# Kernel optimization log

Measured on AMD Instinct MI355X. Metric: run time of the kernel, lower is better.

Reference implementation:

```python
import jax, jax.numpy as jnp
import numpy as np


def setup_inputs() -> dict:
    key = jax.random.key(0)
    kx, kk, kq, kv = jax.random.split(key, 4)
    B, T, C = 4, 2048, 1024
    scale = 1.0 / np.sqrt(C)
    x = jax.random.normal(kx, (B, T, C), dtype=jnp.float32)
    # nn.Linear(C, C, bias=False): y = x @ W.T, W is [C, C]
    Wk = jax.random.normal(kk, (C, C), dtype=jnp.float32) * scale
    Wq = jax.random.normal(kq, (C, C), dtype=jnp.float32) * scale
    Wv = jax.random.normal(kv, (C, C), dtype=jnp.float32) * scale
    return {"x": x, "Wk": Wk, "Wq": Wq, "Wv": Wv}


def reference(x, Wk, Wq, Wv):
    B, T, C = x.shape
    k = jnp.einsum('btc,dc->btd', x, Wk)  # [B,T,C]
    q = jnp.einsum('btc,dc->btd', x, Wq)
    v = jnp.einsum('btc,dc->btd', x, Wv)
    # full T x T score matrix, scaled by C**-0.5 (note: C, not head_dim split)
    wei = jnp.einsum('btd,bsd->bts', q, k) * (C ** -0.5)  # [B,T,T]
    causal = jnp.tril(jnp.ones((T, T), dtype=bool))
    wei = jnp.where(causal, wei, -jnp.inf)
    wei = jax.nn.softmax(wei, axis=-1)
    # dropout(p=0.1) omitted: reference is eval-mode (identity)
    out = jnp.einsum('bts,bsd->btd', wei, v)  # [B,T,C]
    return out
```

## Files before the change

kernel.cpp:

```cpp
#include <hip/hip_runtime.h>
#include <cstdio>
#include <cmath>

#define TSEQ 2048
#define CDIM 1024
#define NBATCH 4

typedef float f32x4 __attribute__((ext_vector_type(4)));
typedef __bf16 bf16x8 __attribute__((ext_vector_type(8)));
typedef unsigned short u16;

__device__ __forceinline__ u16 f2bf(float f) {
  unsigned u = __builtin_bit_cast(unsigned, f);
  unsigned r = (u + 0x7FFFu + ((u >> 16) & 1u)) >> 16;
  return (u16)r;
}

__device__ __forceinline__ void gload_lds16(const void* g, void* l) {
  __builtin_amdgcn_global_load_lds(
      (__attribute__((address_space(1))) void*)g,
      (__attribute__((address_space(3))) void*)l, 16, 0, 0);
}

#define SWZ2(b_) ((b_) ^ ((((b_) >> 7) & 7) << 4))

__device__ __forceinline__ void gemm128(
    const u16* __restrict__ A, const u16* __restrict__ B,
    int lda, int ldb, int m0, int n0, int nT,
    char* smem, f32x4 acc[4][4])
{
  u16* Ab = (u16*)smem;
  u16* Bb = (u16*)(smem + 32768);
  const int tid = threadIdx.x, w = tid >> 6, l = tid & 63;
  const int wr = w >> 1, wc = w & 1;
  const int frow = l & 15, fko = l >> 4;
  const int srow = l >> 3;
  const int scol = ((l & 7) * 8) ^ (((l >> 3) & 7) << 3);

  const u16* gA = A + (size_t)(m0 + w * 32 + srow) * lda + scol;
  const u16* gB = B + (size_t)(n0 + w * 32 + srow) * ldb + scol;

  auto stageA = [&](int t) {
    if (t >= nT) return;
    const u16* s = gA + t * 64;
    u16* d = Ab + (t & 1) * 8192 + w * 2048;
    gload_lds16(s, d);
    gload_lds16(s + (size_t)8 * lda, d + 512);
    gload_lds16(s + (size_t)16 * lda, d + 1024);
    gload_lds16(s + (size_t)24 * lda, d + 1536);
  };
  auto stageB = [&](int t) {
    if (t >= nT) return;
    const u16* s = gB + t * 64;
    u16* d = Bb + (t & 1) * 8192 + w * 2048;
    gload_lds16(s, d);
    gload_lds16(s + (size_t)8 * ldb, d + 512);
    gload_lds16(s + (size_t)16 * ldb, d + 1024);
    gload_lds16(s + (size_t)24 * ldb, d + 1536);
  };

#define AOFF(mf, ks) SWZ2(((wr * 64 + (mf) * 16 + frow) * 128 + (ks) * 64 + fko * 16))
#define BOFF(nf, ks) SWZ2(((wc * 64 + (nf) * 16 + frow) * 128 + (ks) * 64 + fko * 16))

  stageB(0); stageA(0); stageB(1); stageA(1);
  asm volatile("s_waitcnt vmcnt(8)" ::: "memory");
  __builtin_amdgcn_s_barrier();

#pragma unroll 1
  for (int t = 0; t < nT; ++t) {
    const char* Abase = (const char*)Ab + (t & 1) * 16384;
    const char* Bbase = (const char*)Bb + (t & 1) * 16384;
    bf16x8 bfr[4][2], af0[2][2];
#pragma unroll
    for (int nf = 0; nf < 4; ++nf)
#pragma unroll
      for (int ks = 0; ks < 2; ++ks)
        bfr[nf][ks] = *(const bf16x8*)(Bbase + BOFF(nf, ks));
#pragma unroll
    for (int mm = 0; mm < 2; ++mm)
#pragma unroll
      for (int ks = 0; ks < 2; ++ks)
        af0[mm][ks] = *(const bf16x8*)(Abase + AOFF(mm, ks));
    __builtin_amdgcn_sched_barrier(0);
    stageB(t + 2);
    __builtin_amdgcn_s_barrier();
    __builtin_amdgcn_s_setprio(1);
#pragma unroll
    for (int ks = 0; ks < 2; ++ks)
#pragma unroll
      for (int mm = 0; mm < 2; ++mm)
#pragma unroll
        for (int nf = 0; nf < 4; ++nf)
          acc[mm][nf] = __builtin_amdgcn_mfma_f32_16x16x32_bf16(
              af0[mm][ks], bfr[nf][ks], acc[mm][nf], 0, 0, 0);
    __builtin_amdgcn_s_setprio(0);
    __builtin_amdgcn_s_barrier();
    bf16x8 af1[2][2];
#pragma unroll
    for (int mm = 0; mm < 2; ++mm)
#pragma unroll
      for (int ks = 0; ks < 2; ++ks)
        af1[mm][ks] = *(const bf16x8*)(Abase + AOFF(2 + mm, ks));
    __builtin_amdgcn_sched_barrier(0);
    stageA(t + 2);
    __builtin_amdgcn_s_barrier();
    __builtin_amdgcn_s_setprio(1);
#pragma unroll
    for (int ks = 0; ks < 2; ++ks)
#pragma unroll
      for (int mm = 0; mm < 2; ++mm)
#pragma unroll
        for (int nf = 0; nf < 4; ++nf)
          acc[2 + mm][nf] = __builtin_amdgcn_mfma_f32_16x16x32_bf16(
              af1[mm][ks], bfr[nf][ks], acc[2 + mm][nf], 0, 0, 0);
    __builtin_amdgcn_s_setprio(0);
    if (t < nT - 2) asm volatile("s_waitcnt vmcnt(8)" ::: "memory");
    else if (t == nT - 2) asm volatile("s_waitcnt vmcnt(0)" ::: "memory");
    __builtin_amdgcn_s_barrier();
  }
#undef AOFF
#undef BOFF
}

#define ACC_ZERO4(acc)                                  \
  _Pragma("unroll") for (int m_ = 0; m_ < 4; ++m_)      \
  _Pragma("unroll") for (int n_ = 0; n_ < 4; ++n_)      \
      acc[m_][n_] = (f32x4){0.f, 0.f, 0.f, 0.f};

__global__ void __launch_bounds__(256) k_cvt_all(
    const float* __restrict__ x, const float* __restrict__ Wk,
    const float* __restrict__ Wq, const float* __restrict__ Wv,
    u16* __restrict__ xb, u16* __restrict__ wb)
{
  const int NX4 = (NBATCH * TSEQ * CDIM) / 4;
  const int NW4 = (CDIM * CDIM) / 4;
  int g = blockIdx.x * 256 + threadIdx.x;
  const float* src; u16* dst; int i;
  if (g < NX4) { src = x; dst = xb; i = g; }
  else {
    int g2 = g - NX4;
    int w = g2 / NW4; i = g2 - w * NW4;
    src = (w == 0) ? Wk : (w == 1) ? Wq : Wv;
    dst = wb + (size_t)w * CDIM * CDIM;
  }
  float4 v = ((const float4*)src)[i];
  ushort4 o;
  o.x = f2bf(v.x); o.y = f2bf(v.y); o.z = f2bf(v.z); o.w = f2bf(v.w);
  ((ushort4*)dst)[i] = o;
}

__global__ void __launch_bounds__(256, 2) k_gemm_qkv_t(
    const u16* __restrict__ xb, const u16* __restrict__ wb,
    u16* __restrict__ kb, u16* __restrict__ qb, u16* __restrict__ vt)
{
  extern __shared__ char smem[];
  const int id = blockIdx.x;
  const int xcd = id & 7, loc = id >> 3;
  const int mt = xcd * 8 + (loc & 7);
  const int nt = loc >> 3;
  const int m0 = mt * 128, n0g = nt * 128;

  f32x4 acc[4][4];
  ACC_ZERO4(acc);
  gemm128(xb, wb, CDIM, CDIM, m0, n0g, 16, smem, acc);

  const int tid = threadIdx.x, w = tid >> 6, l = tid & 63;
  const int wr = w >> 1, wc = w & 1;
  const int frow = l & 15, fko = l >> 4;
  const int z = n0g >> 10;
  if (z < 2) {
    u16* outp = (z == 0) ? kb : qb;
    const float scale = (z == 1) ? 0.03125f : 1.0f;
    const int r0 = m0 + wr * 64 + fko * 4;
    const int c0 = (n0g & 1023) + wc * 64 + frow;
#pragma unroll
    for (int mf = 0; mf < 4; ++mf)
#pragma unroll
      for (int nf = 0; nf < 4; ++nf) {
        const int r = r0 + mf * 16;
        const int c = c0 + nf * 16;
#pragma unroll
        for (int j = 0; j < 4; ++j)
          outp[(size_t)(r + j) * CDIM + c] = f2bf(acc[mf][nf][j] * scale);
      }
  } else {
    __syncthreads();
    u16* tile = (u16*)smem;
#pragma unroll
    for (int mf = 0; mf < 4; ++mf)
#pragma unroll
      for (int nf = 0; nf < 4; ++nf) {
        const int cl = wc * 64 + nf * 16 + frow;
        const int rl = wr * 64 + mf * 16 + fko * 4;
#pragma unroll
        for (int j = 0; j < 4; ++j)
          tile[cl * 136 + rl + j] = f2bf(acc[mf][nf][j]);
      }
    __syncthreads();
    const int b = m0 >> 11, t0 = m0 & 2047;
    const int c0g = n0g - 2048;
    u16* dst = vt + ((size_t)b * CDIM + c0g) * TSEQ + t0;
#pragma unroll
    for (int it = 0; it < 8; ++it) {
      const int idx = it * 256 + tid;
      const int c = idx >> 4, ch = idx & 15;
      bf16x8 v = *(const bf16x8*)(tile + c * 136 + ch * 8);
      *(bf16x8*)(dst + (size_t)c * TSEQ + ch * 8) = v;
    }
  }
}

__global__ void __launch_bounds__(256, 2) k_gemm_scores_t(
    const u16* __restrict__ qb, const u16* __restrict__ kb,
    u16* __restrict__ pb, float* __restrict__ rs)
{
  extern __shared__ char smem[];
  const int id = blockIdx.x;
  const int sw = (id & 7) * 68 + (id >> 3);
  const int b = sw / 136;
  const int wq = sw - b * 136;
  int y = (int)((sqrtf(8.f * wq + 1.f) - 1.f) * 0.5f);
  while ((y + 1) * (y + 2) / 2 <= wq) ++y;
  while (y * (y + 1) / 2 > wq) --y;
  const int xt = wq - y * (y + 1) / 2;
  const int m0 = y * 128, n0 = xt * 128;

  const u16* A = qb + (size_t)b * TSEQ * CDIM;
  const u16* B = kb + (size_t)b * TSEQ * CDIM;
  u16* P = pb + (size_t)b * TSEQ * TSEQ;

  f32x4 acc[4][4];
  ACC_ZERO4(acc);
  gemm128(A, B, CDIM, CDIM, m0, n0, 16, smem, acc);

  const int tid = threadIdx.x, w = tid >> 6, l = tid & 63;
  const int wr = w >> 1, wc = w & 1;
  const int frow = l & 15, fko = l >> 4;
  float* rowpart = (float*)smem;

#pragma unroll
  for (int mf = 0; mf < 4; ++mf) {
#pragma unroll
    for (int j = 0; j < 4; ++j) {
      const int rloc = wr * 64 + mf * 16 + fko * 4 + j;
      const int rglob = m0 + rloc;
      float p4 = 0.f;
#pragma unroll
      for (int nf = 0; nf < 4; ++nf) {
        const int c = n0 + wc * 64 + nf * 16 + frow;
        float e = (c <= rglob) ? __expf(acc[mf][nf][j]) : 0.f;
        p4 += e;
        P[(size_t)rglob * TSEQ + c] = f2bf(e);
      }
#pragma unroll
      for (int d = 1; d < 16; d <<= 1) p4 += __shfl_xor(p4, d);
      if (frow == 0) rowpart[rloc * 2 + wc] = p4;
    }
  }
  __syncthreads();
  if (tid < 128)
    rs[((size_t)b * 16 + xt) * TSEQ + m0 + tid] =
        rowpart[tid * 2] + rowpart[tid * 2 + 1];
}

__global__ void __launch_bounds__(256, 2) k_gemm_pv_t(
    const u16* __restrict__ pb, const u16* __restrict__ vt,
    const float* __restrict__ rs, float* __restrict__ out)
{
  extern __shared__ char smem[];
  const int id = blockIdx.x;
  const int n = id & 7, loc = id >> 3;
  const int b = loc >> 4, mt = loc & 15;
  const int m0 = mt * 128, n0 = n * 128;
  const int nT = 2 * (mt + 1);

  const u16* A = pb + (size_t)b * TSEQ * TSEQ;
  const u16* B = vt + (size_t)b * CDIM * TSEQ;
  float* O = out + (size_t)b * TSEQ * CDIM;

  f32x4 acc[4][4];
  ACC_ZERO4(acc);
  gemm128(A, B, TSEQ, TSEQ, m0, n0, nT, smem, acc);

  const int tid = threadIdx.x, w = tid >> 6, l = tid & 63;
  const int wr = w >> 1, wc = w & 1;
  const int frow = l & 15, fko = l >> 4;

  __syncthreads();
  float* sinv = (float*)smem;
  if (tid < 128) {
    float s = 0.f;
    const float* p = rs + (size_t)b * 16 * TSEQ + m0 + tid;
    for (int x = 0; x <= mt; ++x) s += p[(size_t)x * TSEQ];
    sinv[tid] = 1.f / s;
  }
  __syncthreads();

#pragma unroll
  for (int mf = 0; mf < 4; ++mf) {
    const int rloc = wr * 64 + mf * 16 + fko * 4;
    const int r = m0 + rloc;
    const float4 iv = *(const float4*)&sinv[rloc];
    const float ivj[4] = {iv.x, iv.y, iv.z, iv.w};
#pragma unroll
    for (int nf = 0; nf < 4; ++nf) {
      const int c = n0 + wc * 64 + nf * 16 + frow;
#pragma unroll
      for (int j = 0; j < 4; ++j)
        O[(size_t)(r + j) * CDIM + c] = acc[mf][nf][j] * ivj[j];
    }
  }
}

extern "C" void kernel_launch(void* const* d_in, const int* in_sizes, int n_in,
                              void* d_out, int out_size, void* d_ws, size_t ws_size,
                              hipStream_t stream) {
  const float* x  = (const float*)d_in[0];
  const float* Wk = (const float*)d_in[1];
  const float* Wq = (const float*)d_in[2];
  const float* Wv = (const float*)d_in[3];
  float* out = (float*)d_out;

  const size_t M = (size_t)NBATCH * TSEQ;

  size_t off = 0;
  auto alloc = [&](size_t bytes) {
    void* p = (char*)d_ws + off;
    off += (bytes + 255) & ~(size_t)255;
    return p;
  };
  u16* xb = (u16*)alloc(M * CDIM * 2);
  u16* wb = (u16*)alloc(3ull * CDIM * CDIM * 2);
  u16* qb = (u16*)alloc(M * CDIM * 2);
  u16* kb = (u16*)alloc(M * CDIM * 2);
  u16* vt = (u16*)alloc(M * CDIM * 2);
  u16* pbuf = (u16*)alloc((size_t)NBATCH * TSEQ * TSEQ * 2);
  float* rs = (float*)alloc((size_t)NBATCH * 16 * TSEQ * 4);
  if (off > ws_size) {
    fprintf(stderr, "kernel_launch: ws too small: need %zu, have %zu\n", off, ws_size);
    return;
  }

  const int NX4 = (NBATCH * TSEQ * CDIM) / 4;
  const int NW4 = (CDIM * CDIM) / 4;
  const int cvtBlocks = (NX4 + 3 * NW4) / 256;

  static_cast<void>(hipFuncSetAttribute(
      reinterpret_cast<const void*>(k_gemm_qkv_t),
      hipFuncAttributeMaxDynamicSharedMemorySize, 65536));
  static_cast<void>(hipFuncSetAttribute(
      reinterpret_cast<const void*>(k_gemm_scores_t),
      hipFuncAttributeMaxDynamicSharedMemorySize, 65536));
  static_cast<void>(hipFuncSetAttribute(
      reinterpret_cast<const void*>(k_gemm_pv_t),
      hipFuncAttributeMaxDynamicSharedMemorySize, 65536));

  k_cvt_all<<<cvtBlocks, 256, 0, stream>>>(x, Wk, Wq, Wv, xb, wb);
  k_gemm_qkv_t<<<1536, 256, 65536, stream>>>(xb, wb, kb, qb, vt);
  k_gemm_scores_t<<<544, 256, 65536, stream>>>(qb, kb, pbuf, rs);
  k_gemm_pv_t<<<512, 256, 65536, stream>>>(pbuf, vt, rs, out);
}
```

Measured before the change: 139.5 us.

## Simplify GEMM main loop and stage epilogue stores through LDS for coalescing

The gemm128 main loop is restructured from two half-phases, each with its own barrier and a prefetch issue, into one phase. Each iteration waits, loads all A and B fragments, runs all 32 MFMAs, then issues both next-tile prefetches after a single barrier. Separately, the QKV projection and scores kernels now write their bf16 outputs into an LDS tile and then store them with 16-byte coalesced vector writes, replacing scattered 2-byte global stores. This adds LDS traffic and extra syncs, and the new loop structure may reduce overlap of global loads with MFMA work.

Measured after the change: 135.9 us. -2.6%, faster.

```diff
diff --git a/kernel.cpp b/kernel.cpp
--- a/kernel.cpp
+++ b/kernel.cpp
@@ -63,60 +63,43 @@
 #define BOFF(nf, ks) SWZ2(((wc * 64 + (nf) * 16 + frow) * 128 + (ks) * 64 + fko * 16))
 
   stageB(0); stageA(0); stageB(1); stageA(1);
-  asm volatile("s_waitcnt vmcnt(8)" ::: "memory");
-  __builtin_amdgcn_s_barrier();
 
 #pragma unroll 1
   for (int t = 0; t < nT; ++t) {
+    if (t < nT - 1) asm volatile("s_waitcnt vmcnt(8)" ::: "memory");
+    else            asm volatile("s_waitcnt vmcnt(0)" ::: "memory");
+    __builtin_amdgcn_s_barrier();
+    __builtin_amdgcn_sched_barrier(0);
+
     const char* Abase = (const char*)Ab + (t & 1) * 16384;
     const char* Bbase = (const char*)Bb + (t & 1) * 16384;
-    bf16x8 bfr[4][2], af0[2][2];
+    bf16x8 bfr[4][2], afr[4][2];
 #pragma unroll
     for (int nf = 0; nf < 4; ++nf)
 #pragma unroll
       for (int ks = 0; ks < 2; ++ks)
         bfr[nf][ks] = *(const bf16x8*)(Bbase + BOFF(nf, ks));
 #pragma unroll
-    for (int mm = 0; mm < 2; ++mm)
+    for (int mf = 0; mf < 4; ++mf)
 #pragma unroll
       for (int ks = 0; ks < 2; ++ks)
-        af0[mm][ks] = *(const bf16x8*)(Abase + AOFF(mm, ks));
+        afr[mf][ks] = *(const bf16x8*)(Abase + AOFF(mf, ks));
+
+    __builtin_amdgcn_s_setprio(1);
+#pragma unroll
+    for (int ks = 0; ks < 2; ++ks)
+#pragma unroll
+      for (int mf = 0; mf < 4; ++mf)
+#pragma unroll
+        for (int nf = 0; nf < 4; ++nf)
+          acc[mf][nf] = __builtin_amdgcn_mfma_f32_16x16x32_bf16(
+              afr[mf][ks], bfr[nf][ks], acc[mf][nf], 0, 0, 0);
+    __builtin_amdgcn_s_setprio(0);
+
+    __builtin_amdgcn_s_barrier();
     __builtin_amdgcn_sched_barrier(0);
     stageB(t + 2);
-    __builtin_amdgcn_s_barrier();
-    __builtin_amdgcn_s_setprio(1);
-#pragma unroll
-    for (int ks = 0; ks < 2; ++ks)
-#pragma unroll
-      for (int mm = 0; mm < 2; ++mm)
-#pragma unroll
-        for (int nf = 0; nf < 4; ++nf)
-          acc[mm][nf] = __builtin_amdgcn_mfma_f32_16x16x32_bf16(
-              af0[mm][ks], bfr[nf][ks], acc[mm][nf], 0, 0, 0);
-    __builtin_amdgcn_s_setprio(0);
-    __builtin_amdgcn_s_barrier();
-    bf16x8 af1[2][2];
-#pragma unroll
-    for (int mm = 0; mm < 2; ++mm)
-#pragma unroll
-      for (int ks = 0; ks < 2; ++ks)
-        af1[mm][ks] = *(const bf16x8*)(Abase + AOFF(2 + mm, ks));
-    __builtin_amdgcn_sched_barrier(0);
     stageA(t + 2);
-    __builtin_amdgcn_s_barrier();
-    __builtin_amdgcn_s_setprio(1);
-#pragma unroll
-    for (int ks = 0; ks < 2; ++ks)
-#pragma unroll
-      for (int mm = 0; mm < 2; ++mm)
-#pragma unroll
-        for (int nf = 0; nf < 4; ++nf)
-          acc[2 + mm][nf] = __builtin_amdgcn_mfma_f32_16x16x32_bf16(
-              af1[mm][ks], bfr[nf][ks], acc[2 + mm][nf], 0, 0, 0);
-    __builtin_amdgcn_s_setprio(0);
-    if (t < nT - 2) asm volatile("s_waitcnt vmcnt(8)" ::: "memory");
-    else if (t == nT - 2) asm volatile("s_waitcnt vmcnt(0)" ::: "memory");
-    __builtin_amdgcn_s_barrier();
   }
 #undef AOFF
 #undef BOFF
@@ -168,24 +151,31 @@
   const int wr = w >> 1, wc = w & 1;
   const int frow = l & 15, fko = l >> 4;
   const int z = n0g >> 10;
+  u16* tile = (u16*)smem;
+  __syncthreads();
   if (z < 2) {
     u16* outp = (z == 0) ? kb : qb;
     const float scale = (z == 1) ? 0.03125f : 1.0f;
-    const int r0 = m0 + wr * 64 + fko * 4;
-    const int c0 = (n0g & 1023) + wc * 64 + frow;
 #pragma unroll
     for (int mf = 0; mf < 4; ++mf)
 #pragma unroll
       for (int nf = 0; nf < 4; ++nf) {
-        const int r = r0 + mf * 16;
-        const int c = c0 + nf * 16;
+        const int rl = wr * 64 + mf * 16 + fko * 4;
+        const int cl = wc * 64 + nf * 16 + frow;
 #pragma unroll
         for (int j = 0; j < 4; ++j)
-          outp[(size_t)(r + j) * CDIM + c] = f2bf(acc[mf][nf][j] * scale);
+          tile[(rl + j) * 136 + cl] = f2bf(acc[mf][nf][j] * scale);
       }
+    __syncthreads();
+    u16* dst = outp + (size_t)m0 * CDIM + (n0g & 1023);
+#pragma unroll
+    for (int it = 0; it < 8; ++it) {
+      const int idx = it * 256 + tid;
+      const int r = idx >> 4, ch = idx & 15;
+      *(bf16x8*)(dst + (size_t)r * CDIM + ch * 8) =
+          *(const bf16x8*)(tile + r * 136 + ch * 8);
+    }
   } else {
-    __syncthreads();
-    u16* tile = (u16*)smem;
 #pragma unroll
     for (int mf = 0; mf < 4; ++mf)
 #pragma unroll
@@ -204,8 +194,8 @@
     for (int it = 0; it < 8; ++it) {
       const int idx = it * 256 + tid;
       const int c = idx >> 4, ch = idx & 15;
-      bf16x8 v = *(const bf16x8*)(tile + c * 136 + ch * 8);
-      *(bf16x8*)(dst + (size_t)c * TSEQ + ch * 8) = v;
+      *(bf16x8*)(dst + (size_t)c * TSEQ + ch * 8) =
+          *(const bf16x8*)(tile + c * 136 + ch * 8);
     }
   }
 }
@@ -236,8 +226,10 @@
   const int tid = threadIdx.x, w = tid >> 6, l = tid & 63;
   const int wr = w >> 1, wc = w & 1;
   const int frow = l & 15, fko = l >> 4;
-  float* rowpart = (float*)smem;
-
+  u16* tile = (u16*)smem;
+  float* rowpart = (float*)(smem + 34816);
+
+  __syncthreads();
 #pragma unroll
   for (int mf = 0; mf < 4; ++mf) {
 #pragma unroll
@@ -247,10 +239,11 @@
       float p4 = 0.f;
 #pragma unroll
       for (int nf = 0; nf < 4; ++nf) {
-        const int c = n0 + wc * 64 + nf * 16 + frow;
+        const int cl = wc * 64 + nf * 16 + frow;
+        const int c = n0 + cl;
         float e = (c <= rglob) ? __expf(acc[mf][nf][j]) : 0.f;
         p4 += e;
-        P[(size_t)rglob * TSEQ + c] = f2bf(e);
+        tile[rloc * 136 + cl] = f2bf(e);
       }
 #pragma unroll
       for (int d = 1; d < 16; d <<= 1) p4 += __shfl_xor(p4, d);
@@ -258,6 +251,14 @@
     }
   }
   __syncthreads();
+  u16* dst = P + (size_t)m0 * TSEQ + n0;
+#pragma unroll
+  for (int it = 0; it < 8; ++it) {
+    const int idx = it * 256 + tid;
+    const int r = idx >> 4, ch = idx & 15;
+    *(bf16x8*)(dst + (size_t)r * TSEQ + ch * 8) =
+        *(const bf16x8*)(tile + r * 136 + ch * 8);
+  }
   if (tid < 128)
     rs[((size_t)b * 16 + xt) * TSEQ + m0 + tid] =
         rowpart[tid * 2] + rowpart[tid * 2 + 1];
```
